# Kernel tuning notes

Measured on AMD Instinct MI355X. Metric: run time of the kernel, lower is better.

Reference implementation:

```python
import jax, jax.numpy as jnp
import numpy as np

E = 1024   # n_embd
H = 16     # n_heads
D = 64     # head_dim
G = 4      # n_kv_groups
F = 4096   # ffn hidden_dim
V = 32000  # vocab
L = 4      # n_layers (all full_attention)
B = 1
T = 2048
ROT = 16   # partial_rotary_factor 0.25 * head_dim 64, rounded to even
EPS = 1e-6
THETA = 10000.0


def rope_tables(seq_len):
    # matches compute_rope_params: inv_freq over even indices of rotary_dim
    inv_freq = 1.0 / (THETA ** (jnp.arange(0, ROT, 2, dtype=jnp.float32) / ROT))
    ang = jnp.arange(seq_len, dtype=jnp.float32)[:, None] * inv_freq[None, :]
    ang = jnp.concatenate([ang, ang], axis=1)  # [T, ROT]
    return jnp.cos(ang), jnp.sin(ang)


def rmsnorm(x, w):
    # torch RMSNorm: x * rsqrt(mean(x^2)+eps) * (1 + weight)
    xf = x.astype(jnp.float32)
    n = xf * jax.lax.rsqrt(jnp.mean(xf * xf, axis=-1, keepdims=True) + EPS)
    return (n * (1.0 + w)).astype(x.dtype)


def apply_rope(x, cos, sin):
    # x: [B, h, T, D]; cos/sin: [1, 1, T, ROT]; partial rotary on first ROT dims
    x_rot, x_pass = x[..., :ROT], x[..., ROT:]
    x1, x2 = x_rot[..., :ROT // 2], x_rot[..., ROT // 2:]
    rotated = jnp.concatenate([-x2, x1], axis=-1)
    return jnp.concatenate([x_rot * cos + rotated * sin, x_pass], axis=-1)


def _forward(tokens, emb, Wq, Wk, Wv, Wo, qn, kn, n1, n2, f1, f2, f3, fn, head):
    cos, sin = rope_tables(T)
    cos = cos[None, None]  # [1,1,T,ROT]
    sin = sin[None, None]
    mask = jnp.triu(jnp.ones((T, T), dtype=bool), k=1)  # True = masked
    scale = D ** -0.5
    x = emb[tokens]  # [B,T,E]

    def block(x, p):
        wq, wk, wv, wo, qw, kw, w1, w2, g1, g2, g3 = p
        h = rmsnorm(x, w1)
        # fused Q + gate projection -> [B,T,H,2D], chunk on last dim
        qg = (h @ wq).reshape(B, T, H, 2 * D)
        q = qg[..., :D].transpose(0, 2, 1, 3)            # [B,H,T,D]
        gate = qg[..., D:].reshape(B, T, H * D)          # [B,T,H*D]
        k = (h @ wk).reshape(B, T, G, D).transpose(0, 2, 1, 3)  # [B,G,T,D]
        v = (h @ wv).reshape(B, T, G, D).transpose(0, 2, 1, 3)
        q = rmsnorm(q, qw)
        k = rmsnorm(k, kw)
        q = apply_rope(q, cos, sin)
        k = apply_rope(k, cos, sin)
        k = jnp.repeat(k, H // G, axis=1)  # GQA expand -> [B,H,T,D]
        v = jnp.repeat(v, H // G, axis=1)
        scores = jnp.einsum('bhqd,bhkd->bhqk', q, k)
        scores = jnp.where(mask, -jnp.inf, scores) * scale
        w = jax.nn.softmax(scores.astype(jnp.float32), axis=-1).astype(q.dtype)
        ctx = jnp.einsum('bhqk,bhkd->bhqd', w, v)
        ctx = ctx.transpose(0, 2, 1, 3).reshape(B, T, H * D)
        ctx = ctx * jax.nn.sigmoid(gate)
        x = x + ctx @ wo
        h2 = rmsnorm(x, w2)
        ff = (jax.nn.silu(h2 @ g1) * (h2 @ g2)) @ g3
        return x + ff, None

    params = (Wq, Wk, Wv, Wo, qn, kn, n1, n2, f1, f2, f3)
    x, _ = jax.lax.scan(block, x, params)
    return rmsnorm(x, fn) @ head  # logits [B,T,V]


def setup_inputs() -> dict:
    key = jax.random.key(0)
    ks = jax.random.split(key, 16)
    s = 0.02
    rn = lambda k, shape, sc=s: jax.random.normal(k, shape, jnp.float32) * sc
    return {
        'tokens': jax.random.randint(ks[0], (B, T), 0, V),
        'emb': rn(ks[1], (V, E)),
        'Wq': rn(ks[2], (L, E, 2 * H * D)),
        'Wk': rn(ks[3], (L, E, G * D)),
        'Wv': rn(ks[4], (L, E, G * D)),
        'Wo': rn(ks[5], (L, H * D, E)),
        'qn': rn(ks[6], (L, D)),
        'kn': rn(ks[7], (L, D)),
        'n1': rn(ks[8], (L, E)),
        'n2': rn(ks[9], (L, E)),
        'f1': rn(ks[10], (L, E, F)),
        'f2': rn(ks[11], (L, E, F)),
        'f3': rn(ks[12], (L, F, E)),
        'fn': rn(ks[13], (E,)),
        'head': rn(ks[14], (E, V)),
    }


def reference(tokens, emb, Wq, Wk, Wv, Wo, qn, kn, n1, n2, f1, f2, f3, fn, head):
    return _forward(tokens, emb, Wq, Wk, Wv, Wo, qn, kn, n1, n2, f1, f2, f3, fn, head)
```

## Files before the change

kernel.cpp:

```cpp
#include <hip/hip_runtime.h>

#define T_LEN 2048
#define E_DIM 1024
#define H_N 16
#define G_N 4
#define D_H 64
#define F_DIM 4096
#define V_SZ 32000
#define L_N 4

typedef __attribute__((ext_vector_type(8))) __bf16 bf16x8;
typedef __attribute__((ext_vector_type(4))) float f32x4;

__device__ __forceinline__ unsigned short f2bf(float f){
  unsigned int u = __float_as_uint(f);
  unsigned int r = (u + 0x7FFFu + ((u >> 16) & 1u)) >> 16;
  return (unsigned short)r;
}

__device__ __forceinline__ float bf2f(unsigned short u){
  return __uint_as_float((unsigned int)u << 16);
}

__device__ __forceinline__ unsigned int packbf(float a, float b){
  return (unsigned int)f2bf(a) | ((unsigned int)f2bf(b) << 16);
}

__device__ __forceinline__ f32x4 mfma16(bf16x8 a, bf16x8 b, f32x4 c){
  return __builtin_amdgcn_mfma_f32_16x16x32_bf16(a, b, c, 0, 0, 0);
}

__device__ __forceinline__ void gl16(const void* g, void* l){
  __builtin_amdgcn_global_load_lds((const __attribute__((address_space(1))) void*)g,
                                   (__attribute__((address_space(3))) void*)l, 16, 0, 0);
}

#define SBAR() __builtin_amdgcn_s_barrier()
#define LGK0() asm volatile("s_waitcnt lgkmcnt(0)" ::: "memory")
#define VMC4() asm volatile("s_waitcnt vmcnt(4)" ::: "memory")
#define VMC0() asm volatile("s_waitcnt vmcnt(0)" ::: "memory")

#define QSCALE 0.1803368801111183f

__global__ __launch_bounds__(256) void embed_k(const float* __restrict__ emb,
                                               const int* __restrict__ tokens,
                                               float* __restrict__ x){
  int t = blockIdx.x;
  int tok = tokens[t];
  const float4* src = (const float4*)(emb + (size_t)tok * E_DIM);
  float4* dst = (float4*)(x + (size_t)t * E_DIM);
  dst[threadIdx.x] = src[threadIdx.x];
}

__global__ __launch_bounds__(256) void transpose_bf16(const float* __restrict__ src,
                                                      unsigned short* __restrict__ dst,
                                                      int R, int C){
  __shared__ float tile[32][33];
  int c0 = blockIdx.x * 32, r0 = blockIdx.y * 32;
  int tx = threadIdx.x & 31, ty = threadIdx.x >> 5;
  for (int i = 0; i < 4; i++){
    int r = ty + i * 8;
    tile[r][tx] = src[(size_t)(r0 + r) * C + c0 + tx];
  }
  __syncthreads();
  for (int i = 0; i < 4; i++){
    int r = ty + i * 8;
    dst[(size_t)(c0 + r) * R + r0 + tx] = f2bf(tile[tx][r]);
  }
}

__device__ __forceinline__ void tr32(const float* __restrict__ src, unsigned short* __restrict__ dst,
                                     int R, int C, int bx, int by, float* tile ){
  int c0 = bx * 32, r0 = by * 32;
  int tx = threadIdx.x & 31, ty = threadIdx.x >> 5;
  for (int i = 0; i < 4; i++){
    int r = ty + i * 8;
    tile[r * 33 + tx] = src[(size_t)(r0 + r) * C + c0 + tx];
  }
  __syncthreads();
  for (int i = 0; i < 4; i++){
    int r = ty + i * 8;
    dst[(size_t)(c0 + r) * R + r0 + tx] = f2bf(tile[tx * 33 + r]);
  }
}

#define PREP_PER_LAYER 15872

__global__ __launch_bounds__(256) void prep_weights(const float* __restrict__ Wq_, const float* __restrict__ Wk_,
                                                    const float* __restrict__ Wv_, const float* __restrict__ Wo_,
                                                    const float* __restrict__ f1_, const float* __restrict__ f2_,
                                                    const float* __restrict__ f3_,
                                                    unsigned short* __restrict__ wt_qkv_,
                                                    unsigned short* __restrict__ wt_o_,
                                                    unsigned short* __restrict__ wt_f12i_,
                                                    unsigned short* __restrict__ wt_f3_){
  __shared__ float sh[1100];
  int id = blockIdx.x;
  const int l = id / PREP_PER_LAYER;
  id -= l * PREP_PER_LAYER;
  const float* Wq = Wq_ + (size_t)l * E_DIM * 2048;
  const float* Wk = Wk_ + (size_t)l * E_DIM * 256;
  const float* Wv = Wv_ + (size_t)l * E_DIM * 256;
  const float* Wo = Wo_ + (size_t)l * E_DIM * E_DIM;
  const float* f1 = f1_ + (size_t)l * E_DIM * F_DIM;
  const float* f2 = f2_ + (size_t)l * E_DIM * F_DIM;
  const float* f3 = f3_ + (size_t)l * F_DIM * E_DIM;
  unsigned short* wt_qkv  = wt_qkv_  + (size_t)l * 2560 * E_DIM;
  unsigned short* wt_o    = wt_o_    + (size_t)l * E_DIM * E_DIM;
  unsigned short* wt_f12i = wt_f12i_ + (size_t)l * 2 * F_DIM * E_DIM;
  unsigned short* wt_f3   = wt_f3_   + (size_t)l * E_DIM * F_DIM;

  if (id < 2048){ tr32(Wq, wt_qkv, 1024, 2048, id & 63, id >> 6, sh); return; }
  id -= 2048;
  if (id < 256){ tr32(Wk, wt_qkv + 2048 * 1024, 1024, 256, id & 7, id >> 3, sh); return; }
  id -= 256;
  if (id < 256){ tr32(Wv, wt_qkv + 2304 * 1024, 1024, 256, id & 7, id >> 3, sh); return; }
  id -= 256;
  if (id < 1024){ tr32(Wo, wt_o, 1024, 1024, id & 31, id >> 5, sh); return; }
  id -= 1024;
  if (id < 4096){ tr32(f3, wt_f3, 4096, 1024, id & 31, id >> 5, sh); return; }
  id -= 4096;
  {
    int q = id & 255, kb = id >> 8;
    float* t1 = sh; float* t2 = sh + 32 * 17;
    int c = threadIdx.x & 15, kk0 = threadIdx.x >> 4;
    for (int p = 0; p < 2; p++){
      int kk = p * 16 + kk0;
      t1[kk * 17 + c] = f1[(size_t)(kb * 32 + kk) * F_DIM + q * 16 + c];
      t2[kk * 17 + c] = f2[(size_t)(kb * 32 + kk) * F_DIM + q * 16 + c];
    }
    __syncthreads();
    int kk = threadIdx.x & 31, rb = threadIdx.x >> 5;
    for (int i = 0; i < 4; i++){
      int r = i * 8 + rb;
      float v = (r < 16) ? t1[kk * 17 + r] : t2[kk * 17 + (r - 16)];
      wt_f12i[(size_t)(q * 32 + r) * 1024 + kb * 32 + kk] = f2bf(v);
    }
  }
}

__global__ __launch_bounds__(256) void rmsnorm_k(const float* __restrict__ x,
                                                 const float* __restrict__ w,
                                                 unsigned short* __restrict__ out){
  const int t = blockIdx.x, tid = threadIdx.x;
  const float4 v = ((const float4*)(x + (size_t)t * E_DIM))[tid];
  float ss = v.x*v.x + v.y*v.y + v.z*v.z + v.w*v.w;
  for (int m = 1; m < 64; m <<= 1) ss += __shfl_xor(ss, m);
  __shared__ float red[4];
  if ((tid & 63) == 0) red[tid >> 6] = ss;
  __syncthreads();
  ss = red[0] + red[1] + red[2] + red[3];
  const float r = rsqrtf(ss * (1.0f / E_DIM) + 1e-6f);
  const float4 wv = ((const float4*)w)[tid];
  ushort4 o;
  o.x = f2bf(v.x * r * (1.0f + wv.x));
  o.y = f2bf(v.y * r * (1.0f + wv.y));
  o.z = f2bf(v.z * r * (1.0f + wv.z));
  o.w = f2bf(v.w * r * (1.0f + wv.w));
  ((ushort4*)(out + (size_t)t * E_DIM))[tid] = o;
}

template<int MODE>
__global__ __launch_bounds__(512) void gemm128(const unsigned short* __restrict__ A,
                                               const unsigned short* __restrict__ Bt,
                                               float* __restrict__ C,
                                               int M, int N, int K,
                                               const float* __restrict__ qn,
                                               const float* __restrict__ kn,
                                               unsigned short* __restrict__ qb,
                                               unsigned short* __restrict__ kb,
                                               unsigned short* __restrict__ vtb,
                                               unsigned short* __restrict__ sg){
  __shared__ unsigned short lds[49152];
  const int tid = threadIdx.x;
  const int lane = tid & 63, w = tid >> 6;
  const int wm = w >> 2, wn = w & 3;
  const int l15 = lane & 15, l4 = lane >> 4;

  const int nwg = gridDim.x;
  const int xcd = (int)blockIdx.x & 7, lin = (int)blockIdx.x >> 3;
  const int q8 = nwg >> 3, r8 = nwg & 7;
  const int wgid = (xcd < r8 ? xcd * (q8 + 1) : r8 * (q8 + 1) + (xcd - r8) * q8) + lin;
  const int nm = M >> 7;
  const int bm = wgid % nm, bn = wgid / nm;
  const int m0 = bm * 128, n0 = bn * 256;

  const int KS = K / gridDim.y;
  const int kbeg = blockIdx.y * KS;
  const int NT = KS >> 6;

  const int srow = (lane >> 3);
  const int scol = lane & 7;

  auto stageA = [&](int b, int kt){
    #pragma unroll
    for (int c = 0; c < 2; c++){
      int r = w * 16 + c * 8 + srow;
      const unsigned short* g = A + (size_t)(m0 + r) * K + kbeg + kt * 64 + ((scol ^ (r & 7)) << 3);
      gl16(g, (char*)lds + b * 16384 + (w * 16 + c * 8) * 128);
    }
  };
  auto stageB = [&](int b, int h, int kt){
    #pragma unroll
    for (int c = 0; c < 2; c++){
      int r = w * 16 + c * 8 + srow;
      const unsigned short* g = Bt + (size_t)(n0 + h * 128 + r) * K + kbeg + kt * 64 + ((scol ^ (r & 7)) << 3);
      gl16(g, (char*)lds + 32768 + (b * 2 + h) * 16384 + (w * 16 + c * 8) * 128);
    }
  };

  const int sl0 = ((l4)     ^ (l15 & 7)) << 4;
  const int sl1 = ((4 | l4) ^ (l15 & 7)) << 4;

  f32x4 acc[4][4] = {};
  bf16x8 aF[8], bF[8];

  stageA(0, 0); stageB(0, 0, 0); stageB(0, 1, 0);
  if (NT > 1){ stageB(1, 0, 1); stageB(1, 1, 1); }
  VMC4();
  SBAR();

  for (int kt = 0; kt < NT; kt++){
    const int buf = kt & 1;
    const char* Ab = (const char*)lds + buf * 16384;
    const char* Bb = (const char*)lds + 32768 + (buf * 2 + (wn >> 1)) * 16384;
    const int brbase = (wn & 1) * 64;

    #pragma unroll
    for (int mf = 0; mf < 4; mf++){
      int r = wm * 64 + mf * 16 + l15;
      aF[mf * 2 + 0] = *(const bf16x8*)(Ab + r * 128 + sl0);
      aF[mf * 2 + 1] = *(const bf16x8*)(Ab + r * 128 + sl1);
    }
    #pragma unroll
    for (int nf = 0; nf < 2; nf++){
      int r = brbase + nf * 16 + l15;
      bF[nf * 2 + 0] = *(const bf16x8*)(Bb + r * 128 + sl0);
      bF[nf * 2 + 1] = *(const bf16x8*)(Bb + r * 128 + sl1);
    }
    if (kt + 1 < NT) stageA(buf ^ 1, kt + 1);
    SBAR(); LGK0();
    __builtin_amdgcn_s_setprio(1);
    #pragma unroll
    for (int mf = 0; mf < 4; mf++)
      #pragma unroll
      for (int nf = 0; nf < 2; nf++){
        acc[mf][nf] = mfma16(aF[mf * 2 + 0], bF[nf * 2 + 0], acc[mf][nf]);
        acc[mf][nf] = mfma16(aF[mf * 2 + 1], bF[nf * 2 + 1], acc[mf][nf]);
      }
    __builtin_amdgcn_s_setprio(0);
    SBAR();

    #pragma unroll
    for (int nf = 2; nf < 4; nf++){
      int r = brbase + nf * 16 + l15;
      bF[nf * 2 + 0] = *(const bf16x8*)(Bb + r * 128 + sl0);
      bF[nf * 2 + 1] = *(const bf16x8*)(Bb + r * 128 + sl1);
    }
    SBAR(); LGK0();
    __builtin_amdgcn_s_setprio(1);
    #pragma unroll
    for (int mf = 0; mf < 4; mf++)
      #pragma unroll
      for (int nf = 2; nf < 4; nf++){
        acc[mf][nf] = mfma16(aF[mf * 2 + 0], bF[nf * 2 + 0], acc[mf][nf]);
        acc[mf][nf] = mfma16(aF[mf * 2 + 1], bF[nf * 2 + 1], acc[mf][nf]);
      }
    __builtin_amdgcn_s_setprio(0);
    SBAR();

    if (kt + 2 < NT){
      stageB(buf, 0, kt + 2);
      stageB(buf, 1, kt + 2);
      VMC4();
    } else {
      VMC0();
    }
    SBAR();
  }

  if (MODE == 0 || MODE == 2){
    #pragma unroll
    for (int mf = 0; mf < 4; mf++)
      #pragma unroll
      for (int nf = 0; nf < 4; nf++){
        int col = n0 + wn * 64 + nf * 16 + l15;
        int row0 = m0 + wm * 64 + mf * 16 + l4 * 4;
        #pragma unroll
        for (int r = 0; r < 4; r++){
          size_t idx = (size_t)(row0 + r) * N + col;
          if (MODE == 0) C[idx] = acc[mf][nf][r];
          else atomicAdd(&C[idx], acc[mf][nf][r]);
        }
      }
  } else {
    const int cbase = n0 + wn * 64;
    if (cbase < 2048){
      const int h = cbase >> 7;
      if ((cbase & 64) == 0){
        const float qw0 = qn[l15], qw1 = qn[16 + l15], qw2 = qn[32 + l15], qw3 = qn[48 + l15];
        const float invf = powf(10000.0f, -(float)(l15 & 7) * 0.125f);
        #pragma unroll
        for (int mf = 0; mf < 4; mf++)
          #pragma unroll
          for (int r = 0; r < 4; r++){
            float ss = 0.0f;
            #pragma unroll
            for (int nf = 0; nf < 4; nf++) ss += acc[mf][nf][r] * acc[mf][nf][r];
            ss += __shfl_xor(ss, 1); ss += __shfl_xor(ss, 2);
            ss += __shfl_xor(ss, 4); ss += __shfl_xor(ss, 8);
            const float rs = rsqrtf(ss * (1.0f / 64.0f) + 1e-6f);
            const int t = m0 + wm * 64 + mf * 16 + l4 * 4 + r;
            const float ang = (float)t * invf;
            const float cc = cosf(ang), sn = sinf(ang);
            float x0 = acc[mf][0][r] * rs * (1.0f + qw0);
            float x1 = acc[mf][1][r] * rs * (1.0f + qw1);
            float x2 = acc[mf][2][r] * rs * (1.0f + qw2);
            float x3 = acc[mf][3][r] * rs * (1.0f + qw3);
            float partner = __shfl_xor(x0, 8);
            float o0 = (l15 < 8) ? (x0 * cc - partner * sn) : (x0 * cc + partner * sn);
            unsigned short* qrow = qb + ((size_t)h * T_LEN + t) * 64;
            qrow[l15]      = f2bf(o0 * QSCALE);
            qrow[16 + l15] = f2bf(x1 * QSCALE);
            qrow[32 + l15] = f2bf(x2 * QSCALE);
            qrow[48 + l15] = f2bf(x3 * QSCALE);
          }
      } else {
        #pragma unroll
        for (int mf = 0; mf < 4; mf++)
          #pragma unroll
          for (int r = 0; r < 4; r++){
            const int t = m0 + wm * 64 + mf * 16 + l4 * 4 + r;
            unsigned short* srow = sg + (size_t)t * 1024 + h * 64;
            #pragma unroll
            for (int nf = 0; nf < 4; nf++)
              srow[nf * 16 + l15] = f2bf(1.0f / (1.0f + __expf(-acc[mf][nf][r])));
          }
      }
    } else if (cbase < 2304){
      const int g = (cbase - 2048) >> 6;
      const float kw0 = kn[l15], kw1 = kn[16 + l15], kw2 = kn[32 + l15], kw3 = kn[48 + l15];
      const float invf = powf(10000.0f, -(float)(l15 & 7) * 0.125f);
      #pragma unroll
      for (int mf = 0; mf < 4; mf++)
        #pragma unroll
        for (int r = 0; r < 4; r++){
          float ss = 0.0f;
          #pragma unroll
          for (int nf = 0; nf < 4; nf++) ss += acc[mf][nf][r] * acc[mf][nf][r];
          ss += __shfl_xor(ss, 1); ss += __shfl_xor(ss, 2);
          ss += __shfl_xor(ss, 4); ss += __shfl_xor(ss, 8);
          const float rs = rsqrtf(ss * (1.0f / 64.0f) + 1e-6f);
          const int t = m0 + wm * 64 + mf * 16 + l4 * 4 + r;
          const float ang = (float)t * invf;
          const float cc = cosf(ang), sn = sinf(ang);
          float x0 = acc[mf][0][r] * rs * (1.0f + kw0);
          float x1 = acc[mf][1][r] * rs * (1.0f + kw1);
          float x2 = acc[mf][2][r] * rs * (1.0f + kw2);
          float x3 = acc[mf][3][r] * rs * (1.0f + kw3);
          float partner = __shfl_xor(x0, 8);
          float o0 = (l15 < 8) ? (x0 * cc - partner * sn) : (x0 * cc + partner * sn);
          unsigned short* krow = kb + ((size_t)g * T_LEN + t) * 64;
          krow[l15]      = f2bf(o0);
          krow[16 + l15] = f2bf(x1);
          krow[32 + l15] = f2bf(x2);
          krow[48 + l15] = f2bf(x3);
        }
    } else {
      const int g = (cbase - 2304) >> 6;
      #pragma unroll
      for (int mf = 0; mf < 4; mf++)
        #pragma unroll
        for (int r = 0; r < 4; r++){
          const int t = m0 + wm * 64 + mf * 16 + l4 * 4 + r;
          #pragma unroll
          for (int nf = 0; nf < 4; nf++)
            vtb[((size_t)g * 64 + nf * 16 + l15) * T_LEN + t] = f2bf(acc[mf][nf][r]);
        }
    }
  }
}

template<int EPI>
__global__ __launch_bounds__(512, 2) void gemm256(const unsigned short* __restrict__ A,
                                                  const unsigned short* __restrict__ Bt,
                                                  float* __restrict__ outF,
                                                  unsigned short* __restrict__ outH,
                                                  int M, int N, int K){
  __shared__ unsigned short lds[65536];
  const int tid = threadIdx.x;
  const int lane = tid & 63, w = tid >> 6;
  const int wm = w >> 2, wn = w & 3;
  const int l15 = lane & 15, l4 = lane >> 4;

  const int nwg = gridDim.x;
  const int xcd = (int)blockIdx.x & 7, lin = (int)blockIdx.x >> 3;
  const int q8 = nwg >> 3, r8 = nwg & 7;
  const int wgid = (xcd < r8 ? xcd * (q8 + 1) : r8 * (q8 + 1) + (xcd - r8) * q8) + lin;
  const int nm = M >> 8;
  const int bm = wgid % nm, bn = wgid / nm;
  const int m0 = bm * 256, n0 = bn * 256;

  const int KS = K / gridDim.y;
  const int kbeg = blockIdx.y * KS;
  const int NT = KS >> 6;

  const int srow = (lane >> 3);
  const int scol = lane & 7;

  auto stageA = [&](int b, int h, int kt){
    #pragma unroll
    for (int c = 0; c < 2; c++){
      int r = w * 16 + c * 8 + srow;
      const unsigned short* g = A + (size_t)(m0 + h * 128 + r) * K + kbeg + kt * 64 + ((scol ^ (r & 7)) << 3);
      gl16(g, (char*)lds + (b * 2 + h) * 16384 + (w * 16 + c * 8) * 128);
    }
  };
  auto stageB = [&](int b, int h, int kt){
    #pragma unroll
    for (int c = 0; c < 2; c++){
      int r = w * 16 + c * 8 + srow;
      const unsigned short* g = Bt + (size_t)(n0 + h * 128 + r) * K + kbeg + kt * 64 + ((scol ^ (r & 7)) << 3);
      gl16(g, (char*)lds + 65536 + (b * 2 + h) * 16384 + (w * 16 + c * 8) * 128);
    }
  };

  const int sl0 = ((l4)     ^ (l15 & 7)) << 4;
  const int sl1 = ((4 | l4) ^ (l15 & 7)) << 4;

  f32x4 acc[8][4] = {};
  bf16x8 aF[8], bF[8];

  stageA(0, 0, 0); stageA(0, 1, 0); stageB(0, 0, 0); stageB(0, 1, 0);
  if (NT > 1){ stageB(1, 0, 1); stageB(1, 1, 1); }
  VMC4();
  SBAR();

  for (int kt = 0; kt < NT; kt++){
    const int buf = kt & 1;
    const char* Ab = (const char*)lds + (buf * 2 + wm) * 16384;
    const char* Bb = (const char*)lds + 65536 + (buf * 2 + (wn >> 1)) * 16384;
    const int brbase = (wn & 1) * 64;

    #pragma unroll
    for (int mf = 0; mf < 4; mf++){
      int r = mf * 16 + l15;
      aF[mf * 2 + 0] = *(const bf16x8*)(Ab + r * 128 + sl0);
      aF[mf * 2 + 1] = *(const bf16x8*)(Ab + r * 128 + sl1);
    }
    #pragma unroll
    for (int nf = 0; nf < 2; nf++){
      int r = brbase + nf * 16 + l15;
      bF[nf * 2 + 0] = *(const bf16x8*)(Bb + r * 128 + sl0);
      bF[nf * 2 + 1] = *(const bf16x8*)(Bb + r * 128 + sl1);
    }
    if (kt + 1 < NT) stageA(buf ^ 1, 0, kt + 1);
    SBAR(); LGK0();
    __builtin_amdgcn_s_setprio(1);
    #pragma unroll
    for (int mf = 0; mf < 4; mf++)
      #pragma unroll
      for (int nf = 0; nf < 2; nf++){
        acc[mf][nf] = mfma16(aF[mf * 2 + 0], bF[nf * 2 + 0], acc[mf][nf]);
        acc[mf][nf] = mfma16(aF[mf * 2 + 1], bF[nf * 2 + 1], acc[mf][nf]);
      }
    __builtin_amdgcn_s_setprio(0);
    SBAR();

    #pragma unroll
    for (int nf = 2; nf < 4; nf++){
      int r = brbase + nf * 16 + l15;
      bF[nf * 2 + 0] = *(const bf16x8*)(Bb + r * 128 + sl0);
      bF[nf * 2 + 1] = *(const bf16x8*)(Bb + r * 128 + sl1);
    }
    if (kt + 1 < NT) stageA(buf ^ 1, 1, kt + 1);
    SBAR(); LGK0();
    __builtin_amdgcn_s_setprio(1);
    #pragma unroll
    for (int mf = 0; mf < 4; mf++)
      #pragma unroll
      for (int nf = 2; nf < 4; nf++){
        acc[mf][nf] = mfma16(aF[mf * 2 + 0], bF[nf * 2 + 0], acc[mf][nf]);
        acc[mf][nf] = mfma16(aF[mf * 2 + 1], bF[nf * 2 + 1], acc[mf][nf]);
      }
    __builtin_amdgcn_s_setprio(0);
    SBAR();

    #pragma unroll
    for (int mf = 0; mf < 4; mf++){
      int r = 64 + mf * 16 + l15;
      aF[mf * 2 + 0] = *(const bf16x8*)(Ab + r * 128 + sl0);
      aF[mf * 2 + 1] = *(const bf16x8*)(Ab + r * 128 + sl1);
    }
    if (kt + 2 < NT) stageB(buf, 0, kt + 2);
    SBAR(); LGK0();
    __builtin_amdgcn_s_setprio(1);
    #pragma unroll
    for (int mf = 0; mf < 4; mf++)
      #pragma unroll
      for (int nf = 2; nf < 4; nf++){
        acc[4 + mf][nf] = mfma16(aF[mf * 2 + 0], bF[nf * 2 + 0], acc[4 + mf][nf]);
        acc[4 + mf][nf] = mfma16(aF[mf * 2 + 1], bF[nf * 2 + 1], acc[4 + mf][nf]);
      }
    __builtin_amdgcn_s_setprio(0);
    SBAR();

    if (kt + 2 < NT) stageB(buf, 1, kt + 2);
    SBAR();
    __builtin_amdgcn_s_setprio(1);
    #pragma unroll
    for (int mf = 0; mf < 4; mf++)
      #pragma unroll
      for (int nf = 0; nf < 2; nf++){
        acc[4 + mf][nf] = mfma16(aF[mf * 2 + 0], bF[nf * 2 + 0], acc[4 + mf][nf]);
        acc[4 + mf][nf] = mfma16(aF[mf * 2 + 1], bF[nf * 2 + 1], acc[4 + mf][nf]);
      }
    __builtin_amdgcn_s_setprio(0);
    if (kt + 2 < NT) { VMC4(); } else { VMC0(); }
    SBAR();
  }

  if (EPI == 0 || EPI == 2){
    #pragma unroll
    for (int mfg = 0; mfg < 8; mfg++){
      #pragma unroll
      for (int nf = 0; nf < 4; nf++){
        int col = n0 + wn * 64 + nf * 16 + l15;
        int row0 = m0 + wm * 128 + mfg * 16 + l4 * 4;
        #pragma unroll
        for (int r = 0; r < 4; r++){
          size_t idx = (size_t)(row0 + r) * N + col;
          if (EPI == 0) outF[idx] = acc[mfg][nf][r];
          else atomicAdd(&outF[idx], acc[mfg][nf][r]);
        }
      }
    }
  } else {
    const int NH = N >> 1;
    #pragma unroll
    for (int mfg = 0; mfg < 8; mfg++){
      #pragma unroll
      for (int nfp = 0; nfp < 2; nfp++){
        int col = (n0 >> 1) + wn * 32 + nfp * 16 + l15;
        int row0 = m0 + wm * 128 + mfg * 16 + l4 * 4;
        #pragma unroll
        for (int r = 0; r < 4; r++){
          float u = acc[mfg][nfp * 2 + 0][r];
          float g = acc[mfg][nfp * 2 + 1][r];
          outH[(size_t)(row0 + r) * NH + col] = f2bf(u / (1.0f + __expf(-u)) * g);
        }
      }
    }
  }
}

__global__ __launch_bounds__(256) void attn_k(const unsigned short* __restrict__ qb,
                                              const unsigned short* __restrict__ kb,
                                              const unsigned short* __restrict__ vt,
                                              const unsigned short* __restrict__ sgate,
                                              unsigned short* __restrict__ ctxg){
  const int qt = blockIdx.x, h = blockIdx.y;
  const int g = h >> 2;
  const int tid = threadIdx.x;
  const int wv = tid >> 6;
  const int lane = tid & 63;
  const int l15 = lane & 15, l4 = lane >> 4;
  const int q0 = qt * 16;
  const int nch = (q0 >> 6) + 1;

  __shared__ unsigned short Pl[4][16][72];
  __shared__ float sO[4][16][66];
  __shared__ float sM[4][16];
  __shared__ float sL[4][16];

  const bf16x8 aq0 = *(const bf16x8*)(qb + ((size_t)h * T_LEN + q0 + l15) * D_H + l4 * 8);
  const bf16x8 aq1 = *(const bf16x8*)(qb + ((size_t)h * T_LEN + q0 + l15) * D_H + 32 + l4 * 8);

  f32x4 acc[4] = {};
  float m = -1e30f, lpart = 0.0f;

  for (int c = wv; c < nch; c += 4){
    const int kv0 = c << 6;
    f32x4 sc[4];
    #pragma unroll
    for (int cp = 0; cp < 4; cp++){
      const unsigned short* kbase = kb + ((size_t)g * T_LEN + kv0 + cp * 16 + l15) * D_H + l4 * 8;
      bf16x8 bk0 = *(const bf16x8*)(kbase);
      bf16x8 bk1 = *(const bf16x8*)(kbase + 32);
      f32x4 z = {0.f, 0.f, 0.f, 0.f};
      z = mfma16(bk0, aq0, z);
      z = mfma16(bk1, aq1, z);
      sc[cp] = z;
    }
    if (c == nch - 1){
      #pragma unroll
      for (int cp = 0; cp < 4; cp++)
        #pragma unroll
        for (int j = 0; j < 4; j++){
          int kv = kv0 + cp * 16 + l4 * 4 + j;
          sc[cp][j] = (kv <= q0 + l15) ? sc[cp][j] : -1e30f;
        }
    }
    float mx = sc[0][0];
    #pragma unroll
    for (int cp = 0; cp < 4; cp++)
      #pragma unroll
      for (int j = 0; j < 4; j++) mx = fmaxf(mx, sc[cp][j]);
    mx = fmaxf(mx, __shfl_xor(mx, 16));
    mx = fmaxf(mx, __shfl_xor(mx, 32));
    const float mnew = fmaxf(m, mx);
    const bool grew = !__all(mnew == m);
    const float mold = m;
    m = mnew;

    float ssum = 0.0f;
    unsigned int up[4][2];
    #pragma unroll
    for (int cp = 0; cp < 4; cp++){
      float p0 = exp2f(sc[cp][0] - mnew);
      float p1 = exp2f(sc[cp][1] - mnew);
      float p2 = exp2f(sc[cp][2] - mnew);
      float p3 = exp2f(sc[cp][3] - mnew);
      ssum += (p0 + p1) + (p2 + p3);
      up[cp][0] = packbf(p0, p1);
      up[cp][1] = packbf(p2, p3);
    }
    if (grew){
      const float resc = exp2f(mold - mnew);
      lpart *= resc;
      float r0 = __shfl(resc, l4 * 4 + 0);
      float r1 = __shfl(resc, l4 * 4 + 1);
      float r2 = __shfl(resc, l4 * 4 + 2);
      float r3 = __shfl(resc, l4 * 4 + 3);
      #pragma unroll
      for (int nt = 0; nt < 4; nt++){
        acc[nt][0] *= r0; acc[nt][1] *= r1; acc[nt][2] *= r2; acc[nt][3] *= r3;
      }
    }
    lpart += ssum;

    #pragma unroll
    for (int cp = 0; cp < 4; cp++){
      uint2 pr; pr.x = up[cp][0]; pr.y = up[cp][1];
      *(uint2*)&Pl[wv][l15][cp * 16 + l4 * 4] = pr;
    }
    asm volatile("s_waitcnt lgkmcnt(0)" ::: "memory");
    const bf16x8 pa0 = *(const bf16x8*)&Pl[wv][l15][l4 * 8];
    const bf16x8 pa1 = *(const bf16x8*)&Pl[wv][l15][32 + l4 * 8];
    #pragma unroll
    for (int nt = 0; nt < 4; nt++){
      const unsigned short* vbase = vt + ((size_t)g * 64 + nt * 16 + l15) * T_LEN + kv0;
      bf16x8 bv0 = *(const bf16x8*)(vbase + l4 * 8);
      bf16x8 bv1 = *(const bf16x8*)(vbase + 32 + l4 * 8);
      acc[nt] = mfma16(pa1, bv1, mfma16(pa0, bv0, acc[nt]));
    }
  }

  lpart += __shfl_xor(lpart, 16);
  lpart += __shfl_xor(lpart, 32);

  #pragma unroll
  for (int j = 0; j < 4; j++){
    int row = l4 * 4 + j;
    #pragma unroll
    for (int nt = 0; nt < 4; nt++)
      sO[wv][row][nt * 16 + l15] = acc[nt][j];
  }
  if (l4 == 0){
    sM[wv][l15] = m;
    sL[wv][l15] = lpart;
  }
  __syncthreads();

  #pragma unroll
  for (int rr = 0; rr < 4; rr++){
    int r = wv * 4 + rr;
    float m0 = sM[0][r], m1 = sM[1][r], m2 = sM[2][r], m3 = sM[3][r];
    float ms = fmaxf(fmaxf(m0, m1), fmaxf(m2, m3));
    float w0 = exp2f(m0 - ms), w1 = exp2f(m1 - ms), w2 = exp2f(m2 - ms), w3 = exp2f(m3 - ms);
    float accv = w0 * sO[0][r][lane] + w1 * sO[1][r][lane] + w2 * sO[2][r][lane] + w3 * sO[3][r][lane];
    float lsum = w0 * sL[0][r] + w1 * sL[1][r] + w2 * sL[2][r] + w3 * sL[3][r];
    float sgv = bf2f(sgate[(size_t)(q0 + r) * 1024 + h * 64 + lane]);
    float val = accv / lsum * sgv;
    ctxg[(size_t)(q0 + r) * (H_N * D_H) + h * D_H + lane] = f2bf(val);
  }
}

extern "C" void kernel_launch(void* const* d_in, const int* in_sizes, int n_in,
                              void* d_out, int out_size, void* d_ws, size_t ws_size,
                              hipStream_t stream){
  (void)in_sizes; (void)n_in; (void)out_size; (void)ws_size;
  const int*   tokens = (const int*)d_in[0];
  const float* emb    = (const float*)d_in[1];
  const float* Wq     = (const float*)d_in[2];
  const float* Wk     = (const float*)d_in[3];
  const float* Wv     = (const float*)d_in[4];
  const float* Wo     = (const float*)d_in[5];
  const float* qn     = (const float*)d_in[6];
  const float* kn     = (const float*)d_in[7];
  const float* n1     = (const float*)d_in[8];
  const float* n2     = (const float*)d_in[9];
  const float* f1     = (const float*)d_in[10];
  const float* f2     = (const float*)d_in[11];
  const float* f3     = (const float*)d_in[12];
  const float* fn     = (const float*)d_in[13];
  const float* head   = (const float*)d_in[14];
  float* out = (float*)d_out;

  char* ws = (char*)d_ws;
  size_t off = 0;
  auto alloc = [&](size_t bytes)->char*{
    char* p = ws + off;
    off += (bytes + 255) & ~(size_t)255;
    return p;
  };
  float*          x        = (float*)alloc((size_t)T_LEN * E_DIM * 4);
  unsigned short* hbf      = (unsigned short*)alloc((size_t)T_LEN * E_DIM * 2);
  unsigned short* qb       = (unsigned short*)alloc((size_t)H_N * T_LEN * D_H * 2);
  unsigned short* kb       = (unsigned short*)alloc((size_t)G_N * T_LEN * D_H * 2);
  unsigned short* vt       = (unsigned short*)alloc((size_t)G_N * D_H * T_LEN * 2);
  unsigned short* sgate    = (unsigned short*)alloc((size_t)T_LEN * E_DIM * 2);
  unsigned short* ctxg     = (unsigned short*)alloc((size_t)T_LEN * E_DIM * 2);
  unsigned short* hg       = (unsigned short*)alloc((size_t)T_LEN * F_DIM * 2);
  unsigned short* wt_qkv4  = (unsigned short*)alloc((size_t)L_N * 2560 * E_DIM * 2);
  unsigned short* wt_o4    = (unsigned short*)alloc((size_t)L_N * E_DIM * E_DIM * 2);
  unsigned short* wt_f12i4 = (unsigned short*)alloc((size_t)L_N * 2 * F_DIM * E_DIM * 2);
  unsigned short* wt_f34   = (unsigned short*)alloc((size_t)L_N * E_DIM * F_DIM * 2);
  unsigned short* wt_head  = (unsigned short*)alloc((size_t)V_SZ * E_DIM * 2);

  embed_k<<<T_LEN, 256, 0, stream>>>(emb, tokens, x);
  transpose_bf16<<<dim3(V_SZ / 32, E_DIM / 32), 256, 0, stream>>>(head, wt_head, E_DIM, V_SZ);
  prep_weights<<<L_N * PREP_PER_LAYER, 256, 0, stream>>>(Wq, Wk, Wv, Wo, f1, f2, f3,
                                                         wt_qkv4, wt_o4, wt_f12i4, wt_f34);

  for (int l = 0; l < L_N; l++){
    const unsigned short* wt_qkv  = wt_qkv4  + (size_t)l * 2560 * E_DIM;
    const unsigned short* wt_o    = wt_o4    + (size_t)l * E_DIM * E_DIM;
    const unsigned short* wt_f12i = wt_f12i4 + (size_t)l * 2 * F_DIM * E_DIM;
    const unsigned short* wt_f3   = wt_f34   + (size_t)l * E_DIM * F_DIM;

    rmsnorm_k<<<T_LEN, 256, 0, stream>>>(x, n1 + l * E_DIM, hbf);
    gemm128<3><<<(T_LEN / 128) * (2560 / 256), 512, 0, stream>>>(hbf, wt_qkv, nullptr, T_LEN, 2560, E_DIM,
                                                                 qn + l * D_H, kn + l * D_H, qb, kb, vt, sgate);
    attn_k<<<dim3(T_LEN / 16, H_N), 256, 0, stream>>>(qb, kb, vt, sgate, ctxg);
    gemm128<2><<<dim3((T_LEN / 128) * (E_DIM / 256), 4), 512, 0, stream>>>(ctxg, wt_o, x, T_LEN, E_DIM, E_DIM,
                                                                           nullptr, nullptr, nullptr, nullptr, nullptr, nullptr);

    rmsnorm_k<<<T_LEN, 256, 0, stream>>>(x, n2 + l * E_DIM, hbf);
    gemm256<1><<<(T_LEN / 256) * (2 * F_DIM / 256), 512, 0, stream>>>(hbf, wt_f12i, nullptr, hg, T_LEN, 2 * F_DIM, E_DIM);
    gemm256<2><<<dim3((T_LEN / 256) * (E_DIM / 256), 8), 512, 0, stream>>>(hg, wt_f3, x, nullptr, T_LEN, E_DIM, F_DIM);
  }

  rmsnorm_k<<<T_LEN, 256, 0, stream>>>(x, fn, hbf);
  gemm256<0><<<(T_LEN / 256) * (V_SZ / 256), 512, 0, stream>>>(hbf, wt_head, out, nullptr, T_LEN, V_SZ, E_DIM);
}
```

Baseline: 1.401 ms.

## Add K32 128x256 GEMM for O-proj and FFN, split head GEMM

Adds a new gemmk32 kernel that uses 128x256 tiles with a K-step of 32, a smaller LDS footprint and simple double buffering. It replaces gemm128 for the output projection and gemm256 for both FFN GEMMs, with split-K atomics kept where they were. The vocab-head GEMM is launched as three column-chunk calls, and the split-K and epilogue template paths are removed from the old kernels. The aim is more resident workgroups and a better spread of work across CUs. The cost is less data reuse per LDS load and a sync on every short K step.

After: 1.470 ms. 1.05x slower.

```diff
diff --git a/kernel.cpp b/kernel.cpp
--- a/kernel.cpp
+++ b/kernel.cpp
@@ -70,7 +70,7 @@
 }
 
 __device__ __forceinline__ void tr32(const float* __restrict__ src, unsigned short* __restrict__ dst,
-                                     int R, int C, int bx, int by, float* tile ){
+                                     int R, int C, int bx, int by, float* tile){
   int c0 = bx * 32, r0 = by * 32;
   int tx = threadIdx.x & 31, ty = threadIdx.x >> 5;
   for (int i = 0; i < 4; i++){
@@ -161,6 +161,113 @@
 }
 
 template<int MODE>
+__global__ __launch_bounds__(512) void gemmk32(const unsigned short* __restrict__ A,
+                                               const unsigned short* __restrict__ Bt,
+                                               float* __restrict__ outF,
+                                               unsigned short* __restrict__ outH,
+                                               int M, int N, int K){
+  __shared__ unsigned short lds[24576];
+  const int tid = threadIdx.x;
+  const int lane = tid & 63, w = tid >> 6;
+  const int wm = w >> 2, wn = w & 3;
+  const int l15 = lane & 15, l4 = lane >> 4;
+
+  const int nwg = gridDim.x;
+  const int xcd = (int)blockIdx.x & 7, lin = (int)blockIdx.x >> 3;
+  const int q8 = nwg >> 3, r8 = nwg & 7;
+  const int wgid = (xcd < r8 ? xcd * (q8 + 1) : r8 * (q8 + 1) + (xcd - r8) * q8) + lin;
+  const int nm = M >> 7;
+  const int bm = wgid % nm, bn = wgid / nm;
+  const int m0 = bm * 128, n0 = bn * 256;
+
+  const int KS = K / gridDim.y;
+  const int kbeg = blockIdx.y * KS;
+  const int NT = KS >> 5;
+
+  const int arow = tid >> 2, aslot = tid & 3;
+  auto stage = [&](int b, int kt){
+    {
+      const unsigned short* g = A + (size_t)(m0 + arow) * K + kbeg + kt * 32 + ((aslot ^ (arow & 3)) << 3);
+      gl16(g, (char*)lds + b * 8192 + tid * 16);
+    }
+    #pragma unroll
+    for (int i = 0; i < 2; i++){
+      int flat = tid + i * 512;
+      int row = flat >> 2, slot = flat & 3;
+      const unsigned short* g = Bt + (size_t)(n0 + row) * K + kbeg + kt * 32 + ((slot ^ (row & 3)) << 3);
+      gl16(g, (char*)lds + 16384 + b * 16384 + flat * 16);
+    }
+  };
+
+  const int rsl = (l4 ^ (l15 & 3)) << 4;
+
+  f32x4 acc[4][4] = {};
+  bf16x8 aF[4], bF[4];
+
+  stage(0, 0);
+  VMC0();
+  SBAR();
+
+  for (int kt = 0; kt < NT; kt++){
+    const int buf = kt & 1;
+    if (kt + 1 < NT) stage(buf ^ 1, kt + 1);
+    const char* Ab = (const char*)lds + buf * 8192;
+    const char* Bb = (const char*)lds + 16384 + buf * 16384;
+    #pragma unroll
+    for (int mf = 0; mf < 4; mf++){
+      int r = wm * 64 + mf * 16 + l15;
+      aF[mf] = *(const bf16x8*)(Ab + r * 64 + rsl);
+    }
+    #pragma unroll
+    for (int nf = 0; nf < 4; nf++){
+      int r = wn * 64 + nf * 16 + l15;
+      bF[nf] = *(const bf16x8*)(Bb + r * 64 + rsl);
+    }
+    LGK0();
+    __builtin_amdgcn_s_setprio(1);
+    #pragma unroll
+    for (int mf = 0; mf < 4; mf++)
+      #pragma unroll
+      for (int nf = 0; nf < 4; nf++)
+        acc[mf][nf] = mfma16(aF[mf], bF[nf], acc[mf][nf]);
+    __builtin_amdgcn_s_setprio(0);
+    VMC0();
+    SBAR();
+  }
+
+  if (MODE == 0 || MODE == 2){
+    #pragma unroll
+    for (int mf = 0; mf < 4; mf++)
+      #pragma unroll
+      for (int nf = 0; nf < 4; nf++){
+        int col = n0 + wn * 64 + nf * 16 + l15;
+        int row0 = m0 + wm * 64 + mf * 16 + l4 * 4;
+        #pragma unroll
+        for (int r = 0; r < 4; r++){
+          size_t idx = (size_t)(row0 + r) * N + col;
+          if (MODE == 0) outF[idx] = acc[mf][nf][r];
+          else atomicAdd(&outF[idx], acc[mf][nf][r]);
+        }
+      }
+  } else {
+    const int NH = N >> 1;
+    #pragma unroll
+    for (int mf = 0; mf < 4; mf++)
+      #pragma unroll
+      for (int nfp = 0; nfp < 2; nfp++){
+        int col = (n0 >> 1) + wn * 32 + nfp * 16 + l15;
+        int row0 = m0 + wm * 64 + mf * 16 + l4 * 4;
+        #pragma unroll
+        for (int r = 0; r < 4; r++){
+          float u = acc[mf][nfp * 2 + 0][r];
+          float g = acc[mf][nfp * 2 + 1][r];
+          outH[(size_t)(row0 + r) * NH + col] = f2bf(u / (1.0f + __expf(-u)) * g);
+        }
+      }
+  }
+}
+
+template<int MODE>
 __global__ __launch_bounds__(512) void gemm128(const unsigned short* __restrict__ A,
                                                const unsigned short* __restrict__ Bt,
                                                float* __restrict__ C,
@@ -185,9 +292,7 @@
   const int bm = wgid % nm, bn = wgid / nm;
   const int m0 = bm * 128, n0 = bn * 256;
 
-  const int KS = K / gridDim.y;
-  const int kbeg = blockIdx.y * KS;
-  const int NT = KS >> 6;
+  const int NT = K >> 6;
 
   const int srow = (lane >> 3);
   const int scol = lane & 7;
@@ -196,7 +301,7 @@
     #pragma unroll
     for (int c = 0; c < 2; c++){
       int r = w * 16 + c * 8 + srow;
-      const unsigned short* g = A + (size_t)(m0 + r) * K + kbeg + kt * 64 + ((scol ^ (r & 7)) << 3);
+      const unsigned short* g = A + (size_t)(m0 + r) * K + kt * 64 + ((scol ^ (r & 7)) << 3);
       gl16(g, (char*)lds + b * 16384 + (w * 16 + c * 8) * 128);
     }
   };
@@ -204,7 +309,7 @@
     #pragma unroll
     for (int c = 0; c < 2; c++){
       int r = w * 16 + c * 8 + srow;
-      const unsigned short* g = Bt + (size_t)(n0 + h * 128 + r) * K + kbeg + kt * 64 + ((scol ^ (r & 7)) << 3);
+      const unsigned short* g = Bt + (size_t)(n0 + h * 128 + r) * K + kt * 64 + ((scol ^ (r & 7)) << 3);
       gl16(g, (char*)lds + 32768 + (b * 2 + h) * 16384 + (w * 16 + c * 8) * 128);
     }
   };
@@ -279,7 +384,7 @@
     SBAR();
   }
 
-  if (MODE == 0 || MODE == 2){
+  if (MODE == 0){
     #pragma unroll
     for (int mf = 0; mf < 4; mf++)
       #pragma unroll
@@ -287,11 +392,8 @@
         int col = n0 + wn * 64 + nf * 16 + l15;
         int row0 = m0 + wm * 64 + mf * 16 + l4 * 4;
         #pragma unroll
-        for (int r = 0; r < 4; r++){
-          size_t idx = (size_t)(row0 + r) * N + col;
-          if (MODE == 0) C[idx] = acc[mf][nf][r];
-          else atomicAdd(&C[idx], acc[mf][nf][r]);
-        }
+        for (int r = 0; r < 4; r++)
+          C[(size_t)(row0 + r) * N + col] = acc[mf][nf][r];
       }
   } else {
     const int cbase = n0 + wn * 64;
@@ -381,11 +483,9 @@
   }
 }
 
-template<int EPI>
 __global__ __launch_bounds__(512, 2) void gemm256(const unsigned short* __restrict__ A,
                                                   const unsigned short* __restrict__ Bt,
                                                   float* __restrict__ outF,
-                                                  unsigned short* __restrict__ outH,
                                                   int M, int N, int K){
   __shared__ unsigned short lds[65536];
   const int tid = threadIdx.x;
@@ -400,10 +500,7 @@
   const int nm = M >> 8;
   const int bm = wgid % nm, bn = wgid / nm;
   const int m0 = bm * 256, n0 = bn * 256;
-
-  const int KS = K / gridDim.y;
-  const int kbeg = blockIdx.y * KS;
-  const int NT = KS >> 6;
+  const int NT = K >> 6;
 
   const int srow = (lane >> 3);
   const int scol = lane & 7;
@@ -412,7 +509,7 @@
     #pragma unroll
     for (int c = 0; c < 2; c++){
       int r = w * 16 + c * 8 + srow;
-      const unsigned short* g = A + (size_t)(m0 + h * 128 + r) * K + kbeg + kt * 64 + ((scol ^ (r & 7)) << 3);
+      const unsigned short* g = A + (size_t)(m0 + h * 128 + r) * K + kt * 64 + ((scol ^ (r & 7)) << 3);
       gl16(g, (char*)lds + (b * 2 + h) * 16384 + (w * 16 + c * 8) * 128);
     }
   };
@@ -420,7 +517,7 @@
     #pragma unroll
     for (int c = 0; c < 2; c++){
       int r = w * 16 + c * 8 + srow;
-      const unsigned short* g = Bt + (size_t)(n0 + h * 128 + r) * K + kbeg + kt * 64 + ((scol ^ (r & 7)) << 3);
+      const unsigned short* g = Bt + (size_t)(n0 + h * 128 + r) * K + kt * 64 + ((scol ^ (r & 7)) << 3);
       gl16(g, (char*)lds + 65536 + (b * 2 + h) * 16384 + (w * 16 + c * 8) * 128);
     }
   };
@@ -520,36 +617,15 @@
     SBAR();
   }
 
-  if (EPI == 0 || EPI == 2){
-    #pragma unroll
-    for (int mfg = 0; mfg < 8; mfg++){
-      #pragma unroll
-      for (int nf = 0; nf < 4; nf++){
-        int col = n0 + wn * 64 + nf * 16 + l15;
-        int row0 = m0 + wm * 128 + mfg * 16 + l4 * 4;
-        #pragma unroll
-        for (int r = 0; r < 4; r++){
-          size_t idx = (size_t)(row0 + r) * N + col;
-          if (EPI == 0) outF[idx] = acc[mfg][nf][r];
-          else atomicAdd(&outF[idx], acc[mfg][nf][r]);
-        }
-      }
-    }
-  } else {
-    const int NH = N >> 1;
-    #pragma unroll
-    for (int mfg = 0; mfg < 8; mfg++){
-      #pragma unroll
-      for (int nfp = 0; nfp < 2; nfp++){
-        int col = (n0 >> 1) + wn * 32 + nfp * 16 + l15;
-        int row0 = m0 + wm * 128 + mfg * 16 + l4 * 4;
-        #pragma unroll
-        for (int r = 0; r < 4; r++){
-          float u = acc[mfg][nfp * 2 + 0][r];
-          float g = acc[mfg][nfp * 2 + 1][r];
-          outH[(size_t)(row0 + r) * NH + col] = f2bf(u / (1.0f + __expf(-u)) * g);
-        }
-      }
+  #pragma unroll
+  for (int mfg = 0; mfg < 8; mfg++){
+    #pragma unroll
+    for (int nf = 0; nf < 4; nf++){
+      int col = n0 + wn * 64 + nf * 16 + l15;
+      int row0 = m0 + wm * 128 + mfg * 16 + l4 * 4;
+      #pragma unroll
+      for (int r = 0; r < 4; r++)
+        outF[(size_t)(row0 + r) * N + col] = acc[mfg][nf][r];
     }
   }
 }
@@ -743,14 +819,17 @@
     gemm128<3><<<(T_LEN / 128) * (2560 / 256), 512, 0, stream>>>(hbf, wt_qkv, nullptr, T_LEN, 2560, E_DIM,
                                                                  qn + l * D_H, kn + l * D_H, qb, kb, vt, sgate);
     attn_k<<<dim3(T_LEN / 16, H_N), 256, 0, stream>>>(qb, kb, vt, sgate, ctxg);
-    gemm128<2><<<dim3((T_LEN / 128) * (E_DIM / 256), 4), 512, 0, stream>>>(ctxg, wt_o, x, T_LEN, E_DIM, E_DIM,
-                                                                           nullptr, nullptr, nullptr, nullptr, nullptr, nullptr);
+    gemmk32<2><<<dim3((T_LEN / 128) * (E_DIM / 256), 4), 512, 0, stream>>>(ctxg, wt_o, x, nullptr, T_LEN, E_DIM, E_DIM);
 
     rmsnorm_k<<<T_LEN, 256, 0, stream>>>(x, n2 + l * E_DIM, hbf);
-    gemm256<1><<<(T_LEN / 256) * (2 * F_DIM / 256), 512, 0, stream>>>(hbf, wt_f12i, nullptr, hg, T_LEN, 2 * F_DIM, E_DIM);
-    gemm256<2><<<dim3((T_LEN / 256) * (E_DIM / 256), 8), 512, 0, stream>>>(hg, wt_f3, x, nullptr, T_LEN, E_DIM, F_DIM);
+    gemmk32<1><<<(T_LEN / 128) * (2 * F_DIM / 256), 512, 0, stream>>>(hbf, wt_f12i, nullptr, hg, T_LEN, 2 * F_DIM, E_DIM);
+    gemmk32<2><<<dim3((T_LEN / 128) * (E_DIM / 256), 8), 512, 0, stream>>>(hg, wt_f3, x, nullptr, T_LEN, E_DIM, F_DIM);
   }
 
   rmsnorm_k<<<T_LEN, 256, 0, stream>>>(x, fn, hbf);
-  gemm256<0><<<(T_LEN / 256) * (V_SZ / 256), 512, 0, stream>>>(hbf, wt_head, out, nullptr, T_LEN, V_SZ, E_DIM);
-}
+  gemm256<<<(T_LEN / 256) * 42, 512, 0, stream>>>(hbf, wt_head, out, T_LEN, V_SZ, E_DIM);
+  gemm256<<<(T_LEN / 256) * 42, 512, 0, stream>>>(hbf, wt_head + (size_t)(42 * 256) * E_DIM,
+                                                  out + (size_t)(42 * 256), T_LEN, V_SZ, E_DIM);
+  gemm256<<<(T_LEN / 256) * 41, 512, 0, stream>>>(hbf, wt_head + (size_t)(84 * 256) * E_DIM,
+                                                  out + (size_t)(84 * 256), T_LEN, V_SZ, E_DIM);
+}
```
